# Optimization experiments

Measured on AMD Instinct MI355X. Metric: run time of the kernel, lower is better.

## Reference

```python
import jax, jax.numpy as jnp
import numpy as np

N, E, F_IN, HD, H, G, NG, OUT = 50000, 800000, 128, 64, 4, 512, 50, 64
HC = HD * H  # 256
LN_EPS = 1e-5

def _lin(k, fi, fo):
    return jax.random.normal(k, (fi, fo), jnp.float32) / np.sqrt(fi).astype(np.float32)

def setup_inputs() -> dict:
    key = jax.random.key(0)
    ks = jax.random.split(key, 26)
    x = jax.random.normal(ks[0], (N, F_IN), jnp.float32)
    edge_index = jax.random.randint(ks[1], (2, E), 0, N)
    batch = jnp.sort(jax.random.randint(ks[2], (N,), 0, G))
    group_ids = jax.random.randint(ks[3], (N,), 0, NG)
    inp = {
        'x': x, 'edge_index': edge_index, 'batch': batch, 'group_ids': group_ids,
        'group_table': jax.random.normal(ks[4], (NG, HD), jnp.float32),
        'inW': _lin(ks[5], F_IN + HD, HD), 'inb': jnp.zeros((HD,), jnp.float32),
        'inln_g': jnp.ones((HD,), jnp.float32), 'inln_b': jnp.zeros((HD,), jnp.float32),
        'W0': _lin(ks[6], HD, HC), 'as0': jax.random.normal(ks[7], (H, HD), jnp.float32) * 0.1,
        'ad0': jax.random.normal(ks[8], (H, HD), jnp.float32) * 0.1, 'b0': jnp.zeros((HC,), jnp.float32),
        'ln0g': jnp.ones((HC,), jnp.float32), 'ln0b': jnp.zeros((HC,), jnp.float32),
        'W1': _lin(ks[9], HC, HC), 'as1': jax.random.normal(ks[10], (H, HD), jnp.float32) * 0.1,
        'ad1': jax.random.normal(ks[11], (H, HD), jnp.float32) * 0.1, 'b1': jnp.zeros((HC,), jnp.float32),
        'ln1g': jnp.ones((HC,), jnp.float32), 'ln1b': jnp.zeros((HC,), jnp.float32),
        'fc1W': _lin(ks[12], HC, HD), 'fc1b': jnp.zeros((HD,), jnp.float32),
        'fc2W': _lin(ks[13], HD, OUT), 'fc2b': jnp.zeros((OUT,), jnp.float32),
    }
    return inp

def _layer_norm(x, g, b):
    mu = jnp.mean(x, axis=-1, keepdims=True)
    var = jnp.mean(jnp.square(x - mu), axis=-1, keepdims=True)
    return (x - mu) * jax.lax.rsqrt(var + LN_EPS) * g + b

def _gat_conv(x, src, dst, W, a_src, a_dst, bias):
    # x: [N, Fin] -> per-head projection [N, H, HD]
    xl = (x @ W).reshape(-1, H, HD)
    al_s = jnp.einsum('nhc,hc->nh', xl, a_src)  # [N, H]
    al_d = jnp.einsum('nhc,hc->nh', xl, a_dst)
    e = jax.nn.leaky_relu(al_s[src] + al_d[dst], 0.2)  # [Etot, H]
    m = jax.ops.segment_max(e, dst, num_segments=N)    # stable softmax over in-edges
    ex = jnp.exp(e - m[dst])
    s = jax.ops.segment_sum(ex, dst, num_segments=N)
    alpha = ex / (s[dst] + 1e-16)
    msg = xl[src] * alpha[:, :, None]                   # [Etot, H, HD]
    out = jax.ops.segment_sum(msg, dst, num_segments=N)
    return out.reshape(-1, HC) + bias

def reference(x, edge_index, batch, group_ids, group_table, inW, inb, inln_g, inln_b,
              W0, as0, ad0, b0, ln0g, ln0b, W1, as1, ad1, b1, ln1g, ln1b,
              fc1W, fc1b, fc2W, fc2b):
    # group embedding concat + input projection (Linear -> LN -> GELU)
    h = jnp.concatenate([x, group_table[group_ids]], axis=-1)
    h = jax.nn.gelu(_layer_norm(h @ inW + inb, inln_g, inln_b), approximate=False)
    # add self-loops (PyG GATConv default)
    loop = jnp.arange(N)
    src = jnp.concatenate([edge_index[0], loop])
    dst = jnp.concatenate([edge_index[1], loop])
    # layer 0: dims 64 -> 256, no residual (width mismatch)
    h = jax.nn.gelu(_layer_norm(_gat_conv(h, src, dst, W0, as0, ad0, b0), ln0g, ln0b), approximate=False)
    # layer 1: 256 -> 256, residual applies
    identity = h
    h = jax.nn.gelu(_layer_norm(_gat_conv(h, src, dst, W1, as1, ad1, b1), ln1g, ln1b), approximate=False)
    h = h + identity
    # global mean pool over graphs
    sums = jax.ops.segment_sum(h, batch, num_segments=G)
    cnt = jax.ops.segment_sum(jnp.ones((N, 1), h.dtype), batch, num_segments=G)
    pooled = sums / jnp.maximum(cnt, 1.0)
    z = jax.nn.gelu(pooled @ fc1W + fc1b, approximate=False)
    logits = z @ fc2W + fc2b
    return jax.nn.log_softmax(logits, axis=1)
```

## Files before the change

kernel.cpp:

```cpp
#include <hip/hip_runtime.h>
#include <math.h>

#define N_NODES 50000
#define N_EDGES 800000
#define ETOT (N_EDGES + N_NODES)
#define F_IN 128
#define HD 64
#define NHEAD 4
#define HC 256
#define NGRAPH 512
#define NOUT 64
#define LN_EPS 1e-5f

typedef __attribute__((ext_vector_type(8))) short bf16x8;
typedef __attribute__((ext_vector_type(4))) float f32x4;
typedef __attribute__((ext_vector_type(2))) float f32x2;

__device__ __forceinline__ float wave_sum(float v) {
#pragma unroll
    for (int m = 1; m < 64; m <<= 1) v += __shfl_xor(v, m, 64);
    return v;
}
__device__ __forceinline__ float wave_max(float v) {
#pragma unroll
    for (int m = 1; m < 64; m <<= 1) v = fmaxf(v, __shfl_xor(v, m, 64));
    return v;
}
__device__ __forceinline__ float red16(float v) {
    v += __shfl_xor(v, 1, 64);
    v += __shfl_xor(v, 2, 64);
    v += __shfl_xor(v, 4, 64);
    v += __shfl_xor(v, 8, 64);
    return v;
}
__device__ __forceinline__ float gelu_exact(float x) {
    return 0.5f * x * (1.0f + erff(x * 0.70710678118654752f));
}
__device__ __forceinline__ unsigned short f2bf(float x) {
    unsigned int u = __float_as_uint(x);
    return (unsigned short)((u + 0x7fffu + ((u >> 16) & 1u)) >> 16);
}
__device__ __forceinline__ float bf2f(unsigned short u) {
    return __uint_as_float(((unsigned int)u) << 16);
}

__global__ void k_count(const int* __restrict__ ei, int* __restrict__ deg) {
    int t = blockIdx.x * blockDim.x + threadIdx.x;
    if (t >= ETOT) return;
    int dst = (t < N_EDGES) ? ei[N_EDGES + t] : (t - N_EDGES);
    atomicAdd(deg + dst, 1);
}

__global__ void k_scan(const int* __restrict__ deg, int* __restrict__ rowptr,
                       int* __restrict__ cursor) {
    __shared__ int wsum[16];
    __shared__ int chunk_total;
    int tid = threadIdx.x, wid = tid >> 6, lane = tid & 63;
    int carry = 0;
    if (tid == 0) rowptr[0] = 0;
    for (int base = 0; base < N_NODES; base += 1024) {
        int i = base + tid;
        int v = (i < N_NODES) ? deg[i] : 0;
        int incl = v;
#pragma unroll
        for (int off = 1; off < 64; off <<= 1) {
            int t = __shfl_up(incl, off, 64);
            if (lane >= off) incl += t;
        }
        if (lane == 63) wsum[wid] = incl;
        __syncthreads();
        if (wid == 0) {
            int wv = (lane < 16) ? wsum[lane] : 0;
            int wincl = wv;
#pragma unroll
            for (int off = 1; off < 16; off <<= 1) {
                int t = __shfl_up(wincl, off, 64);
                if (lane >= off) wincl += t;
            }
            if (lane < 16) wsum[lane] = wincl - wv;
            if (lane == 15) chunk_total = wincl;
        }
        __syncthreads();
        int total_incl = carry + wsum[wid] + incl;
        if (i < N_NODES) {
            rowptr[i + 1] = total_incl;
            cursor[i] = total_incl - v;
        }
        carry += chunk_total;
        __syncthreads();
    }
}

__global__ void k_fill(const int* __restrict__ ei, int* __restrict__ cursor,
                       int* __restrict__ csr) {
    int t = blockIdx.x * blockDim.x + threadIdx.x;
    if (t >= ETOT) return;
    int src, dst;
    if (t < N_EDGES) { src = ei[t]; dst = ei[N_EDGES + t]; }
    else             { src = t - N_EDGES; dst = src; }
    int p = atomicAdd(cursor + dst, 1);
    csr[p] = src;
}

__global__ void k_prep(const float* __restrict__ x, const int* __restrict__ gid,
                       const float* __restrict__ gt, unsigned short* __restrict__ Ain) {
    int wid = threadIdx.x >> 6, lane = threadIdx.x & 63;
    int node = blockIdx.x * 4 + wid;
    float f0 = x[node * F_IN + lane];
    float f1 = x[node * F_IN + 64 + lane];
    int g = gid[node];
    float f2 = gt[g * HD + lane];
    unsigned short* r = Ain + (size_t)node * 192;
    r[lane] = f2bf(f0);
    r[64 + lane] = f2bf(f1);
    r[128 + lane] = f2bf(f2);
}

__global__ void k_pack(const float* __restrict__ W, unsigned short* __restrict__ out,
                       int K, int N) {
    int tid = blockIdx.x * blockDim.x + threadIdx.x;
    int NB = N >> 4;
    int total = (K >> 5) * NB * 512;
    if (tid >= total) return;
    int i = tid & 7;
    int l = (tid >> 3) & 63;
    int t2 = tid >> 9;
    int nb = t2 % NB;
    int kt = t2 / NB;
    int k = kt * 32 + ((l >> 4) << 3) + i;
    int n = nb * 16 + (l & 15);
    out[tid] = f2bf(W[k * N + n]);
}

__global__ void k_prep_u(const float* __restrict__ W0, const float* __restrict__ as_,
                         const float* __restrict__ ad_, float* __restrict__ us,
                         float* __restrict__ ud) {
    int t = threadIdx.x;
    int h = t >> 6, k = t & 63;
    float ss = 0.f, dd = 0.f;
    for (int c = 0; c < 64; c++) {
        float w = W0[k * 256 + h * 64 + c];
        ss += w * as_[h * 64 + c];
        dd += w * ad_[h * 64 + c];
    }
    us[t] = ss;
    ud[t] = dd;
}

__global__ void k_proj_in_mma(const unsigned short* __restrict__ A,
                              const unsigned short* __restrict__ Wpk,
                              const float* __restrict__ inb, const float* __restrict__ lng,
                              const float* __restrict__ lnb, const float* __restrict__ us,
                              const float* __restrict__ ud, unsigned short* __restrict__ h0bf,
                              float* __restrict__ als0, float* __restrict__ ald0) {
    int wid = threadIdx.x >> 6, lane = threadIdx.x & 63;
    int m0 = blockIdx.x * 64 + wid * 16;
    if (m0 >= N_NODES) return;
    int g16 = lane >> 4, c16 = lane & 15;
    f32x4 acc[4] = {{0,0,0,0},{0,0,0,0},{0,0,0,0},{0,0,0,0}};
#pragma unroll
    for (int kt = 0; kt < 6; kt++) {
        bf16x8 a = *(const bf16x8*)(A + (size_t)(m0 + c16) * 192 + kt * 32 + g16 * 8);
#pragma unroll
        for (int nt = 0; nt < 4; nt++) {
            bf16x8 b = *(const bf16x8*)(Wpk + (((kt * 4 + nt) * 64 + lane) << 3));
            acc[nt] = __builtin_amdgcn_mfma_f32_16x16x32_bf16(a, b, acc[nt], 0, 0, 0);
        }
    }
    float bv[4], gv[4], bb[4];
    float usl[4][4], udl[4][4];
#pragma unroll
    for (int nt = 0; nt < 4; nt++) {
        int c = nt * 16 + c16;
        bv[nt] = inb[c]; gv[nt] = lng[c]; bb[nt] = lnb[c];
#pragma unroll
        for (int h = 0; h < 4; h++) {
            usl[h][nt] = us[h * 64 + c];
            udl[h][nt] = ud[h * 64 + c];
        }
    }
#pragma unroll
    for (int j = 0; j < 4; j++) {
        float d[4], s = 0.f;
#pragma unroll
        for (int nt = 0; nt < 4; nt++) { d[nt] = acc[nt][j] + bv[nt]; s += d[nt]; }
        float mu = red16(s) * (1.0f / 64.0f);
        float v = 0.f;
#pragma unroll
        for (int nt = 0; nt < 4; nt++) { d[nt] -= mu; v += d[nt] * d[nt]; }
        float r = rsqrtf(red16(v) * (1.0f / 64.0f) + LN_EPS);
        int row = m0 + g16 * 4 + j;
        float ps0 = 0, ps1 = 0, ps2 = 0, ps3 = 0;
        float pd0 = 0, pd1 = 0, pd2 = 0, pd3 = 0;
#pragma unroll
        for (int nt = 0; nt < 4; nt++) {
            float y = gelu_exact(d[nt] * r * gv[nt] + bb[nt]);
            unsigned short yb = f2bf(y);
            h0bf[(size_t)row * 64 + nt * 16 + c16] = yb;
            float yr = bf2f(yb);
            ps0 += yr * usl[0][nt]; ps1 += yr * usl[1][nt];
            ps2 += yr * usl[2][nt]; ps3 += yr * usl[3][nt];
            pd0 += yr * udl[0][nt]; pd1 += yr * udl[1][nt];
            pd2 += yr * udl[2][nt]; pd3 += yr * udl[3][nt];
        }
        ps0 = red16(ps0); ps1 = red16(ps1); ps2 = red16(ps2); ps3 = red16(ps3);
        pd0 = red16(pd0); pd1 = red16(pd1); pd2 = red16(pd2); pd3 = red16(pd3);
        if (c16 == 0) {
            float4 s4 = {ps0, ps1, ps2, ps3};
            float4 d4 = {pd0, pd1, pd2, pd3};
            ((float4*)als0)[row] = s4;
            ((float4*)ald0)[row] = d4;
        }
    }
}

__global__ void k_agg0(const int* __restrict__ rowptr, const int* __restrict__ csr,
                       const unsigned short* __restrict__ h0bf, const float* __restrict__ als,
                       const float* __restrict__ ald, unsigned short* __restrict__ aggbf) {
    __shared__ float4 lacc[2][64];
    __shared__ float lss[2][4];
    int wid = threadIdx.x >> 6, lane = threadIdx.x & 63;
    int nloc = wid >> 1, half = wid & 1;
    int node = blockIdx.x * 2 + nloc;
    int start = rowptr[node], end = rowptr[node + 1];
    int g = lane >> 4, l16 = lane & 15;
    float4 adv = ((const float4*)ald)[node];
    int cntE = end - start;
    int mid = start + ((cntE + 1) >> 1);
    int k0 = half ? mid : start;
    int k1 = half ? end : mid;
    float a00 = 0, a01 = 0, a02 = 0, a03 = 0;
    float a10 = 0, a11 = 0, a12 = 0, a13 = 0;
    float a20 = 0, a21 = 0, a22 = 0, a23 = 0;
    float a30 = 0, a31 = 0, a32 = 0, a33 = 0;
    float s0 = 0, s1 = 0, s2 = 0, s3 = 0;
    const ushort4* h04 = (const ushort4*)h0bf;
    for (int kb = k0; kb < k1; kb += 4) {
        int e = kb + g;
        if (e < k1) {
            int sn = csr[e];
            float4 av = ((const float4*)als)[sn];
            float e0 = av.x + adv.x; e0 = fmaxf(e0, 0.2f * e0);
            float e1 = av.y + adv.y; e1 = fmaxf(e1, 0.2f * e1);
            float e2 = av.z + adv.z; e2 = fmaxf(e2, 0.2f * e2);
            float e3 = av.w + adv.w; e3 = fmaxf(e3, 0.2f * e3);
            float w0 = __expf(e0), w1 = __expf(e1), w2 = __expf(e2), w3 = __expf(e3);
            s0 += w0; s1 += w1; s2 += w2; s3 += w3;
            ushort4 hv = h04[(size_t)sn * 16 + l16];
            float x0 = bf2f(hv.x), x1 = bf2f(hv.y), x2 = bf2f(hv.z), x3 = bf2f(hv.w);
            a00 += w0 * x0; a01 += w0 * x1; a02 += w0 * x2; a03 += w0 * x3;
            a10 += w1 * x0; a11 += w1 * x1; a12 += w1 * x2; a13 += w1 * x3;
            a20 += w2 * x0; a21 += w2 * x1; a22 += w2 * x2; a23 += w2 * x3;
            a30 += w3 * x0; a31 += w3 * x1; a32 += w3 * x2; a33 += w3 * x3;
        }
    }
#define RED2(v) v += __shfl_xor(v, 16, 64); v += __shfl_xor(v, 32, 64)
    RED2(a00); RED2(a01); RED2(a02); RED2(a03);
    RED2(a10); RED2(a11); RED2(a12); RED2(a13);
    RED2(a20); RED2(a21); RED2(a22); RED2(a23);
    RED2(a30); RED2(a31); RED2(a32); RED2(a33);
    RED2(s0);  RED2(s1);  RED2(s2);  RED2(s3);
#undef RED2
    if (half) {
        float o0 = (g == 0) ? a00 : (g == 1) ? a10 : (g == 2) ? a20 : a30;
        float o1 = (g == 0) ? a01 : (g == 1) ? a11 : (g == 2) ? a21 : a31;
        float o2 = (g == 0) ? a02 : (g == 1) ? a12 : (g == 2) ? a22 : a32;
        float o3 = (g == 0) ? a03 : (g == 1) ? a13 : (g == 2) ? a23 : a33;
        float4 o = {o0, o1, o2, o3};
        lacc[nloc][lane] = o;
        if (lane < 4) {
            float sv = (lane == 0) ? s0 : (lane == 1) ? s1 : (lane == 2) ? s2 : s3;
            lss[nloc][lane] = sv;
        }
    }
    __syncthreads();
    if (!half) {
        float4 p0 = lacc[nloc][0 + l16];
        float4 p1 = lacc[nloc][16 + l16];
        float4 p2 = lacc[nloc][32 + l16];
        float4 p3 = lacc[nloc][48 + l16];
        a00 += p0.x; a01 += p0.y; a02 += p0.z; a03 += p0.w;
        a10 += p1.x; a11 += p1.y; a12 += p1.z; a13 += p1.w;
        a20 += p2.x; a21 += p2.y; a22 += p2.z; a23 += p2.w;
        a30 += p3.x; a31 += p3.y; a32 += p3.z; a33 += p3.w;
        s0 += lss[nloc][0]; s1 += lss[nloc][1];
        s2 += lss[nloc][2]; s3 += lss[nloc][3];
        float o0 = (g == 0) ? a00 : (g == 1) ? a10 : (g == 2) ? a20 : a30;
        float o1 = (g == 0) ? a01 : (g == 1) ? a11 : (g == 2) ? a21 : a31;
        float o2 = (g == 0) ? a02 : (g == 1) ? a12 : (g == 2) ? a22 : a32;
        float o3 = (g == 0) ? a03 : (g == 1) ? a13 : (g == 2) ? a23 : a33;
        float sg = (g == 0) ? s0 : (g == 1) ? s1 : (g == 2) ? s2 : s3;
        float inv = 1.0f / (sg + 1e-16f);
        ushort4 o = {f2bf(o0 * inv), f2bf(o1 * inv), f2bf(o2 * inv), f2bf(o3 * inv)};
        ((ushort4*)aggbf)[(size_t)node * 64 + lane] = o;
    }
}

__global__ void k_postgemm0(const unsigned short* __restrict__ A,
                            const unsigned short* __restrict__ Wpk,
                            const float* __restrict__ bias, const float* __restrict__ lng,
                            const float* __restrict__ lnb, unsigned short* __restrict__ h1bf) {
    int wid = threadIdx.x >> 6, lane = threadIdx.x & 63;
    int m0 = blockIdx.x * 64 + wid * 16;
    if (m0 >= N_NODES) return;
    int g16 = lane >> 4, c16 = lane & 15;
    f32x4 acc[16] = {};
#pragma unroll
    for (int h = 0; h < 4; h++) {
#pragma unroll
        for (int kt = 0; kt < 2; kt++) {
            bf16x8 a = *(const bf16x8*)(A + (size_t)(m0 + c16) * 256 + h * 64 + kt * 32 + g16 * 8);
#pragma unroll
            for (int nt = 0; nt < 4; nt++) {
                bf16x8 b = *(const bf16x8*)(Wpk + (((kt * 16 + h * 4 + nt) * 64 + lane) << 3));
                acc[h * 4 + nt] = __builtin_amdgcn_mfma_f32_16x16x32_bf16(a, b, acc[h * 4 + nt], 0, 0, 0);
            }
        }
    }
    float bv[16], gv[16], bb[16];
#pragma unroll
    for (int q = 0; q < 16; q++) {
        int c = q * 16 + c16;
        bv[q] = bias[c]; gv[q] = lng[c]; bb[q] = lnb[c];
    }
#pragma unroll
    for (int j = 0; j < 4; j++) {
        float d[16], ssum = 0.f;
#pragma unroll
        for (int q = 0; q < 16; q++) { d[q] = acc[q][j] + bv[q]; ssum += d[q]; }
        float mu = red16(ssum) * (1.0f / 256.0f);
        float v = 0.f;
#pragma unroll
        for (int q = 0; q < 16; q++) { d[q] -= mu; v += d[q] * d[q]; }
        float r = rsqrtf(red16(v) * (1.0f / 256.0f) + LN_EPS);
        int row = m0 + g16 * 4 + j;
#pragma unroll
        for (int q = 0; q < 16; q++) {
            float y = gelu_exact(d[q] * r * gv[q] + bb[q]);
            h1bf[(size_t)row * 256 + q * 16 + c16] = f2bf(y);
        }
    }
}

__global__ void k_proj_mma(const unsigned short* __restrict__ A,
                           const unsigned short* __restrict__ Wpk,
                           const float* __restrict__ as_, const float* __restrict__ ad_,
                           unsigned int* __restrict__ xl8, float* __restrict__ als,
                           float* __restrict__ ald) {
    int wid = threadIdx.x >> 6, lane = threadIdx.x & 63;
    int m0 = blockIdx.x * 16;
    int g16 = lane >> 4, c16 = lane & 15;
    f32x4 acc[4] = {{0,0,0,0},{0,0,0,0},{0,0,0,0},{0,0,0,0}};
#pragma unroll
    for (int kt = 0; kt < 8; kt++) {
        bf16x8 a = *(const bf16x8*)(A + (size_t)(m0 + c16) * 256 + kt * 32 + g16 * 8);
#pragma unroll
        for (int nt = 0; nt < 4; nt++) {
            bf16x8 b = *(const bf16x8*)(Wpk + (((kt * 16 + wid * 4 + nt) * 64 + lane) << 3));
            acc[nt] = __builtin_amdgcn_mfma_f32_16x16x32_bf16(a, b, acc[nt], 0, 0, 0);
        }
    }
    float asv[4], adv[4];
#pragma unroll
    for (int nt = 0; nt < 4; nt++) {
        int c = wid * 64 + nt * 16 + c16;
        asv[nt] = as_[c]; adv[nt] = ad_[c];
    }
#pragma unroll
    for (int j = 0; j < 4; j++) {
        int row = m0 + g16 * 4 + j;
        float v0 = acc[0][j], v1 = acc[1][j], v2 = acc[2][j], v3 = acc[3][j];
        int u = __builtin_amdgcn_cvt_pk_fp8_f32(v0, v1, 0, false);
        u = __builtin_amdgcn_cvt_pk_fp8_f32(v2, v3, u, true);
        xl8[(size_t)row * 64 + wid * 16 + c16] = (unsigned int)u;
        float ps = v0 * asv[0] + v1 * asv[1] + v2 * asv[2] + v3 * asv[3];
        float pd = v0 * adv[0] + v1 * adv[1] + v2 * adv[2] + v3 * adv[3];
        ps = red16(ps); pd = red16(pd);
        if (c16 == 0) { als[row * 4 + wid] = ps; ald[row * 4 + wid] = pd; }
    }
}

__global__ void k_agg1(const int* __restrict__ rowptr, const int* __restrict__ csr,
                       const unsigned int* __restrict__ xl8, const float* __restrict__ als,
                       const float* __restrict__ ald, const float* __restrict__ bias,
                       const float* __restrict__ lng, const float* __restrict__ lnb,
                       const unsigned short* __restrict__ identity_bf,
                       const int* __restrict__ batch, float* __restrict__ pooled,
                       int* __restrict__ cnt) {
    __shared__ float4 lacc[2][64];
    __shared__ float lss[2][64];
    __shared__ float4 lyout[2][64];
    __shared__ int lbatch[2];
    int wid = threadIdx.x >> 6, lane = threadIdx.x & 63;
    int nloc = wid >> 1, half = wid & 1;
    int node = blockIdx.x * 2 + nloc;
    int start = rowptr[node], end = rowptr[node + 1];
    int head = lane >> 4, c16 = lane & 15;
    int fb = head * 64 + c16;
    float adh = ald[node * 4 + head];
    int cntE = end - start;
    int mid = start + ((cntE + 1) >> 1);
    int k0 = half ? mid : start;
    int k1 = half ? end : mid;
    float4 acc = {0.f, 0.f, 0.f, 0.f};
    float s = 0.f;
    int k = k0;
    for (; k + 4 <= k1; k += 4) {
        int sn0 = csr[k], sn1 = csr[k + 1], sn2 = csr[k + 2], sn3 = csr[k + 3];
        float e0 = als[sn0 * 4 + head] + adh;
        float e1 = als[sn1 * 4 + head] + adh;
        float e2 = als[sn2 * 4 + head] + adh;
        float e3 = als[sn3 * 4 + head] + adh;
        unsigned int u0 = xl8[(size_t)sn0 * 64 + lane];
        unsigned int u1 = xl8[(size_t)sn1 * 64 + lane];
        unsigned int u2 = xl8[(size_t)sn2 * 64 + lane];
        unsigned int u3 = xl8[(size_t)sn3 * 64 + lane];
        e0 = fmaxf(e0, 0.2f * e0); e1 = fmaxf(e1, 0.2f * e1);
        e2 = fmaxf(e2, 0.2f * e2); e3 = fmaxf(e3, 0.2f * e3);
        float a0 = __expf(e0), a1 = __expf(e1), a2 = __expf(e2), a3 = __expf(e3);
        s += a0 + a1 + a2 + a3;
        f32x2 lo0 = __builtin_amdgcn_cvt_pk_f32_fp8((int)u0, false);
        f32x2 hi0 = __builtin_amdgcn_cvt_pk_f32_fp8((int)u0, true);
        f32x2 lo1 = __builtin_amdgcn_cvt_pk_f32_fp8((int)u1, false);
        f32x2 hi1 = __builtin_amdgcn_cvt_pk_f32_fp8((int)u1, true);
        f32x2 lo2 = __builtin_amdgcn_cvt_pk_f32_fp8((int)u2, false);
        f32x2 hi2 = __builtin_amdgcn_cvt_pk_f32_fp8((int)u2, true);
        f32x2 lo3 = __builtin_amdgcn_cvt_pk_f32_fp8((int)u3, false);
        f32x2 hi3 = __builtin_amdgcn_cvt_pk_f32_fp8((int)u3, true);
        acc.x += a0 * lo0.x + a1 * lo1.x + a2 * lo2.x + a3 * lo3.x;
        acc.y += a0 * lo0.y + a1 * lo1.y + a2 * lo2.y + a3 * lo3.y;
        acc.z += a0 * hi0.x + a1 * hi1.x + a2 * hi2.x + a3 * hi3.x;
        acc.w += a0 * hi0.y + a1 * hi1.y + a2 * hi2.y + a3 * hi3.y;
    }
    for (; k < k1; k++) {
        int sn = csr[k];
        float e = als[sn * 4 + head] + adh;
        e = fmaxf(e, 0.2f * e);
        float a = __expf(e);
        s += a;
        unsigned int u = xl8[(size_t)sn * 64 + lane];
        f32x2 lo = __builtin_amdgcn_cvt_pk_f32_fp8((int)u, false);
        f32x2 hi = __builtin_amdgcn_cvt_pk_f32_fp8((int)u, true);
        acc.x += a * lo.x; acc.y += a * lo.y;
        acc.z += a * hi.x; acc.w += a * hi.y;
    }
    if (half) { lacc[nloc][lane] = acc; lss[nloc][lane] = s; }
    __syncthreads();
    if (!half) {
        float4 p = lacc[nloc][lane];
        acc.x += p.x; acc.y += p.y; acc.z += p.z; acc.w += p.w;
        s += lss[nloc][lane];
        float inv = 1.0f / (s + 1e-16f);
        acc.x = acc.x * inv + bias[fb];
        acc.y = acc.y * inv + bias[fb + 16];
        acc.z = acc.z * inv + bias[fb + 32];
        acc.w = acc.w * inv + bias[fb + 48];
        float mu = wave_sum(acc.x + acc.y + acc.z + acc.w) * (1.0f / 256.0f);
        float dx = acc.x - mu, dy = acc.y - mu, dz = acc.z - mu, dw = acc.w - mu;
        float var = wave_sum(dx * dx + dy * dy + dz * dz + dw * dw) * (1.0f / 256.0f);
        float r = rsqrtf(var + LN_EPS);
        float g0v = lng[fb], g1v = lng[fb + 16], g2v = lng[fb + 32], g3v = lng[fb + 48];
        float b0v = lnb[fb], b1v = lnb[fb + 16], b2v = lnb[fb + 32], b3v = lnb[fb + 48];
        const unsigned short* idp = identity_bf + (size_t)node * 256 + fb;
        float4 y;
        y.x = gelu_exact(dx * r * g0v + b0v) + bf2f(idp[0]);
        y.y = gelu_exact(dy * r * g1v + b1v) + bf2f(idp[16]);
        y.z = gelu_exact(dz * r * g2v + b2v) + bf2f(idp[32]);
        y.w = gelu_exact(dw * r * g3v + b3v) + bf2f(idp[48]);
        lyout[nloc][lane] = y;
        if (lane == 0) lbatch[nloc] = batch[node];
    }
    __syncthreads();
    if (wid == 0) {
        int g0 = lbatch[0], g1 = lbatch[1];
        float4 a = lyout[0][lane], b = lyout[1][lane];
        float* p0 = pooled + (size_t)g0 * 256 + fb;
        if (g0 == g1) {
            atomicAdd(p0 +  0, a.x + b.x); atomicAdd(p0 + 16, a.y + b.y);
            atomicAdd(p0 + 32, a.z + b.z); atomicAdd(p0 + 48, a.w + b.w);
            if (lane == 0) atomicAdd(cnt + g0, 2);
        } else {
            float* p1 = pooled + (size_t)g1 * 256 + fb;
            atomicAdd(p0 +  0, a.x); atomicAdd(p0 + 16, a.y);
            atomicAdd(p0 + 32, a.z); atomicAdd(p0 + 48, a.w);
            atomicAdd(p1 +  0, b.x); atomicAdd(p1 + 16, b.y);
            atomicAdd(p1 + 32, b.z); atomicAdd(p1 + 48, b.w);
            if (lane == 0) { atomicAdd(cnt + g0, 1); atomicAdd(cnt + g1, 1); }
        }
    }
}

__global__ void k_final(const float* __restrict__ pooled, const int* __restrict__ cnt,
                        const float* __restrict__ fc1W, const float* __restrict__ fc1b,
                        const float* __restrict__ fc2W, const float* __restrict__ fc2b,
                        float* __restrict__ out) {
    __shared__ float prow[4][256];
    __shared__ float zrow[4][64];
    int wid = threadIdx.x >> 6, lane = threadIdx.x & 63;
    int g = blockIdx.x * 4 + wid;
    float inv = 1.0f / fmaxf((float)cnt[g], 1.0f);
#pragma unroll
    for (int k = lane; k < 256; k += 64) prow[wid][k] = pooled[g * 256 + k] * inv;
    __syncthreads();
    float acc = fc1b[lane];
#pragma unroll 4
    for (int k = 0; k < 256; k++) acc += prow[wid][k] * fc1W[k * 64 + lane];
    zrow[wid][lane] = gelu_exact(acc);
    __syncthreads();
    float logit = fc2b[lane];
#pragma unroll 4
    for (int k = 0; k < 64; k++) logit += zrow[wid][k] * fc2W[k * 64 + lane];
    float mx = wave_max(logit);
    float se = wave_sum(__expf(logit - mx));
    out[g * NOUT + lane] = logit - mx - logf(se);
}

extern "C" void kernel_launch(void* const* d_in, const int* in_sizes, int n_in,
                              void* d_out, int out_size, void* d_ws, size_t ws_size,
                              hipStream_t stream) {
    const float* x     = (const float*)d_in[0];
    const int*   ei    = (const int*)d_in[1];
    const int*   batch = (const int*)d_in[2];
    const int*   gid   = (const int*)d_in[3];
    const float* gt    = (const float*)d_in[4];
    const float* inW   = (const float*)d_in[5];
    const float* inb   = (const float*)d_in[6];
    const float* inlng = (const float*)d_in[7];
    const float* inlnb = (const float*)d_in[8];
    const float* W0    = (const float*)d_in[9];
    const float* as0   = (const float*)d_in[10];
    const float* ad0   = (const float*)d_in[11];
    const float* b0    = (const float*)d_in[12];
    const float* ln0g  = (const float*)d_in[13];
    const float* ln0b  = (const float*)d_in[14];
    const float* W1    = (const float*)d_in[15];
    const float* as1   = (const float*)d_in[16];
    const float* ad1   = (const float*)d_in[17];
    const float* b1    = (const float*)d_in[18];
    const float* ln1g  = (const float*)d_in[19];
    const float* ln1b  = (const float*)d_in[20];
    const float* fc1W  = (const float*)d_in[21];
    const float* fc1b  = (const float*)d_in[22];
    const float* fc2W  = (const float*)d_in[23];
    const float* fc2b  = (const float*)d_in[24];
    float* out = (float*)d_out;

    char* ws = (char*)d_ws;
    size_t off = 0;
    auto alloc = [&](size_t bytes) {
        void* p = ws + off;
        off += (bytes + 255) / 256 * 256;
        return p;
    };
    unsigned short* Ain    = (unsigned short*)alloc((size_t)N_NODES * 192 * 2);
    unsigned short* h0bf   = (unsigned short*)alloc((size_t)N_NODES * 64 * 2);
    unsigned short* agg0bf = (unsigned short*)alloc((size_t)N_NODES * 256 * 2);
    unsigned short* h1bf   = (unsigned short*)alloc((size_t)N_NODES * 256 * 2);
    unsigned int*   xl8    = (unsigned int*)alloc((size_t)N_NODES * 64 * 4);
    unsigned short* inWpk  = (unsigned short*)alloc((size_t)192 * 64 * 2);
    unsigned short* W0pk   = (unsigned short*)alloc((size_t)64 * 256 * 2);
    unsigned short* W1pk   = (unsigned short*)alloc((size_t)256 * 256 * 2);
    float* us     = (float*)alloc((size_t)256 * 4);
    float* ud     = (float*)alloc((size_t)256 * 4);
    float* als0   = (float*)alloc((size_t)N_NODES * 4 * 4);
    float* ald0   = (float*)alloc((size_t)N_NODES * 4 * 4);
    float* als1   = (float*)alloc((size_t)N_NODES * 4 * 4);
    float* ald1   = (float*)alloc((size_t)N_NODES * 4 * 4);
    int*   rowptr = (int*)alloc((size_t)(N_NODES + 1) * 4);
    int*   cursor = (int*)alloc((size_t)N_NODES * 4);
    int*   csr    = (int*)alloc((size_t)ETOT * 4);
    float* pooled = (float*)alloc((size_t)NGRAPH * 256 * 4);
    int*   cnt    = (int*)alloc((size_t)NGRAPH * 4);
    int*   deg    = (int*)alloc((size_t)N_NODES * 4);
    size_t zspan = ((char*)deg + (size_t)N_NODES * 4) - (char*)pooled;

    hipMemsetAsync(pooled, 0, zspan, stream);

    int eb = (ETOT + 255) / 256;
    k_count<<<eb, 256, 0, stream>>>(ei, deg);
    k_scan<<<1, 1024, 0, stream>>>(deg, rowptr, cursor);
    k_fill<<<eb, 256, 0, stream>>>(ei, cursor, csr);

    k_prep<<<N_NODES / 4, 256, 0, stream>>>(x, gid, gt, Ain);
    k_pack<<<(192 * 64 + 255) / 256, 256, 0, stream>>>(inW, inWpk, 192, 64);
    k_pack<<<(64 * 256 + 255) / 256, 256, 0, stream>>>(W0, W0pk, 64, 256);
    k_pack<<<(256 * 256 + 255) / 256, 256, 0, stream>>>(W1, W1pk, 256, 256);
    k_prep_u<<<1, 256, 0, stream>>>(W0, as0, ad0, us, ud);

    k_proj_in_mma<<<(N_NODES + 63) / 64, 256, 0, stream>>>(Ain, inWpk, inb, inlng, inlnb,
                                                           us, ud, h0bf, als0, ald0);
    k_agg0<<<N_NODES / 2, 256, 0, stream>>>(rowptr, csr, h0bf, als0, ald0, agg0bf);
    k_postgemm0<<<(N_NODES + 63) / 64, 256, 0, stream>>>(agg0bf, W0pk, b0, ln0g, ln0b, h1bf);
    k_proj_mma<<<N_NODES / 16, 256, 0, stream>>>(h1bf, W1pk, as1, ad1, xl8, als1, ald1);
    k_agg1<<<N_NODES / 2, 256, 0, stream>>>(rowptr, csr, xl8, als1, ald1, b1, ln1g, ln1b,
                                            h1bf, batch, pooled, cnt);
    k_final<<<NGRAPH / 4, 256, 0, stream>>>(pooled, cnt, fc1W, fc1b, fc2W, fc2b, out);
}
```

Before: 426.4 us.

## Store layer-0 features in fp8, merge weight packing kernels, unroll aggregations

```diff
diff --git a/kernel.cpp b/kernel.cpp
--- a/kernel.cpp
+++ b/kernel.cpp
@@ -116,42 +116,54 @@
     r[128 + lane] = f2bf(f2);
 }
 
-__global__ void k_pack(const float* __restrict__ W, unsigned short* __restrict__ out,
-                       int K, int N) {
-    int tid = blockIdx.x * blockDim.x + threadIdx.x;
-    int NB = N >> 4;
-    int total = (K >> 5) * NB * 512;
-    if (tid >= total) return;
-    int i = tid & 7;
-    int l = (tid >> 3) & 63;
-    int t2 = tid >> 9;
-    int nb = t2 % NB;
-    int kt = t2 / NB;
-    int k = kt * 32 + ((l >> 4) << 3) + i;
-    int n = nb * 16 + (l & 15);
-    out[tid] = f2bf(W[k * N + n]);
-}
-
-__global__ void k_prep_u(const float* __restrict__ W0, const float* __restrict__ as_,
-                         const float* __restrict__ ad_, float* __restrict__ us,
-                         float* __restrict__ ud) {
-    int t = threadIdx.x;
-    int h = t >> 6, k = t & 63;
-    float ss = 0.f, dd = 0.f;
-    for (int c = 0; c < 64; c++) {
-        float w = W0[k * 256 + h * 64 + c];
-        ss += w * as_[h * 64 + c];
-        dd += w * ad_[h * 64 + c];
-    }
-    us[t] = ss;
-    ud[t] = dd;
+__global__ void k_pack_all(const float* __restrict__ inW, const float* __restrict__ W0,
+                           const float* __restrict__ W1, const float* __restrict__ as0,
+                           const float* __restrict__ ad0,
+                           unsigned short* __restrict__ inWpk, unsigned short* __restrict__ W0pk,
+                           unsigned short* __restrict__ W1pk, float* __restrict__ us,
+                           float* __restrict__ ud) {
+    int b = blockIdx.x;
+    if (b < 48) {
+        int tid = b * 256 + threadIdx.x;
+        int i = tid & 7, l = (tid >> 3) & 63, t2 = tid >> 9;
+        int nb = t2 % 4, kt = t2 / 4;
+        int k = kt * 32 + ((l >> 4) << 3) + i;
+        int n = nb * 16 + (l & 15);
+        inWpk[tid] = f2bf(inW[k * 64 + n]);
+    } else if (b < 112) {
+        int tid = (b - 48) * 256 + threadIdx.x;
+        int i = tid & 7, l = (tid >> 3) & 63, t2 = tid >> 9;
+        int nb = t2 % 16, kt = t2 / 16;
+        int q = kt * 32 + ((l >> 4) << 3) + i;
+        int k = 16 * (q & 3) + (q >> 2);
+        int n = nb * 16 + (l & 15);
+        W0pk[tid] = f2bf(W0[k * 256 + n]);
+    } else if (b < 368) {
+        int tid = (b - 112) * 256 + threadIdx.x;
+        int i = tid & 7, l = (tid >> 3) & 63, t2 = tid >> 9;
+        int nb = t2 % 16, kt = t2 / 16;
+        int k = kt * 32 + ((l >> 4) << 3) + i;
+        int n = nb * 16 + (l & 15);
+        W1pk[tid] = f2bf(W1[k * 256 + n]);
+    } else {
+        int t = threadIdx.x;
+        int h = t >> 6, k2 = t & 63;
+        float ss = 0.f, dd = 0.f;
+        for (int c = 0; c < 64; c++) {
+            float w = W0[k2 * 256 + h * 64 + c];
+            ss += w * as0[h * 64 + c];
+            dd += w * ad0[h * 64 + c];
+        }
+        us[t] = ss;
+        ud[t] = dd;
+    }
 }
 
 __global__ void k_proj_in_mma(const unsigned short* __restrict__ A,
                               const unsigned short* __restrict__ Wpk,
                               const float* __restrict__ inb, const float* __restrict__ lng,
                               const float* __restrict__ lnb, const float* __restrict__ us,
-                              const float* __restrict__ ud, unsigned short* __restrict__ h0bf,
+                              const float* __restrict__ ud, unsigned int* __restrict__ h08,
                               float* __restrict__ als0, float* __restrict__ ald0) {
     int wid = threadIdx.x >> 6, lane = threadIdx.x & 63;
     int m0 = blockIdx.x * 64 + wid * 16;
@@ -190,19 +202,21 @@
         for (int nt = 0; nt < 4; nt++) { d[nt] -= mu; v += d[nt] * d[nt]; }
         float r = rsqrtf(red16(v) * (1.0f / 64.0f) + LN_EPS);
         int row = m0 + g16 * 4 + j;
-        float ps0 = 0, ps1 = 0, ps2 = 0, ps3 = 0;
-        float pd0 = 0, pd1 = 0, pd2 = 0, pd3 = 0;
-#pragma unroll
-        for (int nt = 0; nt < 4; nt++) {
-            float y = gelu_exact(d[nt] * r * gv[nt] + bb[nt]);
-            unsigned short yb = f2bf(y);
-            h0bf[(size_t)row * 64 + nt * 16 + c16] = yb;
-            float yr = bf2f(yb);
-            ps0 += yr * usl[0][nt]; ps1 += yr * usl[1][nt];
-            ps2 += yr * usl[2][nt]; ps3 += yr * usl[3][nt];
-            pd0 += yr * udl[0][nt]; pd1 += yr * udl[1][nt];
-            pd2 += yr * udl[2][nt]; pd3 += yr * udl[3][nt];
-        }
+        float y0 = gelu_exact(d[0] * r * gv[0] + bb[0]);
+        float y1 = gelu_exact(d[1] * r * gv[1] + bb[1]);
+        float y2 = gelu_exact(d[2] * r * gv[2] + bb[2]);
+        float y3 = gelu_exact(d[3] * r * gv[3] + bb[3]);
+        int u = __builtin_amdgcn_cvt_pk_fp8_f32(y0, y1, 0, false);
+        u = __builtin_amdgcn_cvt_pk_fp8_f32(y2, y3, u, true);
+        h08[(size_t)row * 16 + c16] = (unsigned int)u;
+        float ps0 = y0 * usl[0][0] + y1 * usl[0][1] + y2 * usl[0][2] + y3 * usl[0][3];
+        float ps1 = y0 * usl[1][0] + y1 * usl[1][1] + y2 * usl[1][2] + y3 * usl[1][3];
+        float ps2 = y0 * usl[2][0] + y1 * usl[2][1] + y2 * usl[2][2] + y3 * usl[2][3];
+        float ps3 = y0 * usl[3][0] + y1 * usl[3][1] + y2 * usl[3][2] + y3 * usl[3][3];
+        float pd0 = y0 * udl[0][0] + y1 * udl[0][1] + y2 * udl[0][2] + y3 * udl[0][3];
+        float pd1 = y0 * udl[1][0] + y1 * udl[1][1] + y2 * udl[1][2] + y3 * udl[1][3];
+        float pd2 = y0 * udl[2][0] + y1 * udl[2][1] + y2 * udl[2][2] + y3 * udl[2][3];
+        float pd3 = y0 * udl[3][0] + y1 * udl[3][1] + y2 * udl[3][2] + y3 * udl[3][3];
         ps0 = red16(ps0); ps1 = red16(ps1); ps2 = red16(ps2); ps3 = red16(ps3);
         pd0 = red16(pd0); pd1 = red16(pd1); pd2 = red16(pd2); pd3 = red16(pd3);
         if (c16 == 0) {
@@ -215,7 +229,7 @@
 }
 
 __global__ void k_agg0(const int* __restrict__ rowptr, const int* __restrict__ csr,
-                       const unsigned short* __restrict__ h0bf, const float* __restrict__ als,
+                       const unsigned int* __restrict__ h08, const float* __restrict__ als,
                        const float* __restrict__ ald, unsigned short* __restrict__ aggbf) {
     __shared__ float4 lacc[2][64];
     __shared__ float lss[2][4];
@@ -234,25 +248,43 @@
     float a20 = 0, a21 = 0, a22 = 0, a23 = 0;
     float a30 = 0, a31 = 0, a32 = 0, a33 = 0;
     float s0 = 0, s1 = 0, s2 = 0, s3 = 0;
-    const ushort4* h04 = (const ushort4*)h0bf;
-    for (int kb = k0; kb < k1; kb += 4) {
-        int e = kb + g;
-        if (e < k1) {
-            int sn = csr[e];
-            float4 av = ((const float4*)als)[sn];
-            float e0 = av.x + adv.x; e0 = fmaxf(e0, 0.2f * e0);
-            float e1 = av.y + adv.y; e1 = fmaxf(e1, 0.2f * e1);
-            float e2 = av.z + adv.z; e2 = fmaxf(e2, 0.2f * e2);
-            float e3 = av.w + adv.w; e3 = fmaxf(e3, 0.2f * e3);
-            float w0 = __expf(e0), w1 = __expf(e1), w2 = __expf(e2), w3 = __expf(e3);
-            s0 += w0; s1 += w1; s2 += w2; s3 += w3;
-            ushort4 hv = h04[(size_t)sn * 16 + l16];
-            float x0 = bf2f(hv.x), x1 = bf2f(hv.y), x2 = bf2f(hv.z), x3 = bf2f(hv.w);
-            a00 += w0 * x0; a01 += w0 * x1; a02 += w0 * x2; a03 += w0 * x3;
-            a10 += w1 * x0; a11 += w1 * x1; a12 += w1 * x2; a13 += w1 * x3;
-            a20 += w2 * x0; a21 += w2 * x1; a22 += w2 * x2; a23 += w2 * x3;
-            a30 += w3 * x0; a31 += w3 * x1; a32 += w3 * x2; a33 += w3 * x3;
-        }
+    const float4* als4 = (const float4*)als;
+    for (int kb = k0; kb < k1; kb += 8) {
+        int eA = kb + g, eB = kb + 4 + g;
+        int cA = (eA < k1) ? eA : (k1 - 1);
+        int cB = (eB < k1) ? eB : (k1 - 1);
+        int snA = csr[cA], snB = csr[cB];
+        float4 avA = als4[snA], avB = als4[snB];
+        unsigned int uA = h08[(size_t)snA * 16 + l16];
+        unsigned int uB = h08[(size_t)snB * 16 + l16];
+        float eA0 = avA.x + adv.x; eA0 = fmaxf(eA0, 0.2f * eA0);
+        float eA1 = avA.y + adv.y; eA1 = fmaxf(eA1, 0.2f * eA1);
+        float eA2 = avA.z + adv.z; eA2 = fmaxf(eA2, 0.2f * eA2);
+        float eA3 = avA.w + adv.w; eA3 = fmaxf(eA3, 0.2f * eA3);
+        float wA0 = __expf(eA0), wA1 = __expf(eA1), wA2 = __expf(eA2), wA3 = __expf(eA3);
+        if (eA >= k1) { wA0 = 0.f; wA1 = 0.f; wA2 = 0.f; wA3 = 0.f; }
+        f32x2 loA = __builtin_amdgcn_cvt_pk_f32_fp8((int)uA, false);
+        f32x2 hiA = __builtin_amdgcn_cvt_pk_f32_fp8((int)uA, true);
+        s0 += wA0; s1 += wA1; s2 += wA2; s3 += wA3;
+        float x0 = loA.x, x1 = loA.y, x2 = hiA.x, x3 = hiA.y;
+        a00 += wA0 * x0; a01 += wA0 * x1; a02 += wA0 * x2; a03 += wA0 * x3;
+        a10 += wA1 * x0; a11 += wA1 * x1; a12 += wA1 * x2; a13 += wA1 * x3;
+        a20 += wA2 * x0; a21 += wA2 * x1; a22 += wA2 * x2; a23 += wA2 * x3;
+        a30 += wA3 * x0; a31 += wA3 * x1; a32 += wA3 * x2; a33 += wA3 * x3;
+        float eB0 = avB.x + adv.x; eB0 = fmaxf(eB0, 0.2f * eB0);
+        float eB1 = avB.y + adv.y; eB1 = fmaxf(eB1, 0.2f * eB1);
+        float eB2 = avB.z + adv.z; eB2 = fmaxf(eB2, 0.2f * eB2);
+        float eB3 = avB.w + adv.w; eB3 = fmaxf(eB3, 0.2f * eB3);
+        float wB0 = __expf(eB0), wB1 = __expf(eB1), wB2 = __expf(eB2), wB3 = __expf(eB3);
+        if (eB >= k1) { wB0 = 0.f; wB1 = 0.f; wB2 = 0.f; wB3 = 0.f; }
+        f32x2 loB = __builtin_amdgcn_cvt_pk_f32_fp8((int)uB, false);
+        f32x2 hiB = __builtin_amdgcn_cvt_pk_f32_fp8((int)uB, true);
+        s0 += wB0; s1 += wB1; s2 += wB2; s3 += wB3;
+        float z0 = loB.x, z1 = loB.y, z2 = hiB.x, z3 = hiB.y;
+        a00 += wB0 * z0; a01 += wB0 * z1; a02 += wB0 * z2; a03 += wB0 * z3;
+        a10 += wB1 * z0; a11 += wB1 * z1; a12 += wB1 * z2; a13 += wB1 * z3;
+        a20 += wB2 * z0; a21 += wB2 * z1; a22 += wB2 * z2; a23 += wB2 * z3;
+        a30 += wB3 * z0; a31 += wB3 * z1; a32 += wB3 * z2; a33 += wB3 * z3;
     }
 #define RED2(v) v += __shfl_xor(v, 16, 64); v += __shfl_xor(v, 32, 64)
     RED2(a00); RED2(a01); RED2(a02); RED2(a03);
@@ -405,6 +437,52 @@
     float4 acc = {0.f, 0.f, 0.f, 0.f};
     float s = 0.f;
     int k = k0;
+    for (; k + 8 <= k1; k += 8) {
+        int sn0 = csr[k],     sn1 = csr[k + 1], sn2 = csr[k + 2], sn3 = csr[k + 3];
+        int sn4 = csr[k + 4], sn5 = csr[k + 5], sn6 = csr[k + 6], sn7 = csr[k + 7];
+        float e0 = als[sn0 * 4 + head], e1 = als[sn1 * 4 + head];
+        float e2 = als[sn2 * 4 + head], e3 = als[sn3 * 4 + head];
+        float e4 = als[sn4 * 4 + head], e5 = als[sn5 * 4 + head];
+        float e6 = als[sn6 * 4 + head], e7 = als[sn7 * 4 + head];
+        unsigned int u0 = xl8[(size_t)sn0 * 64 + lane], u1 = xl8[(size_t)sn1 * 64 + lane];
+        unsigned int u2 = xl8[(size_t)sn2 * 64 + lane], u3 = xl8[(size_t)sn3 * 64 + lane];
+        unsigned int u4 = xl8[(size_t)sn4 * 64 + lane], u5 = xl8[(size_t)sn5 * 64 + lane];
+        unsigned int u6 = xl8[(size_t)sn6 * 64 + lane], u7 = xl8[(size_t)sn7 * 64 + lane];
+        e0 += adh; e1 += adh; e2 += adh; e3 += adh;
+        e0 = fmaxf(e0, 0.2f * e0); e1 = fmaxf(e1, 0.2f * e1);
+        e2 = fmaxf(e2, 0.2f * e2); e3 = fmaxf(e3, 0.2f * e3);
+        float a0 = __expf(e0), a1 = __expf(e1), a2 = __expf(e2), a3 = __expf(e3);
+        s += a0 + a1 + a2 + a3;
+        f32x2 lo0 = __builtin_amdgcn_cvt_pk_f32_fp8((int)u0, false);
+        f32x2 hi0 = __builtin_amdgcn_cvt_pk_f32_fp8((int)u0, true);
+        f32x2 lo1 = __builtin_amdgcn_cvt_pk_f32_fp8((int)u1, false);
+        f32x2 hi1 = __builtin_amdgcn_cvt_pk_f32_fp8((int)u1, true);
+        f32x2 lo2 = __builtin_amdgcn_cvt_pk_f32_fp8((int)u2, false);
+        f32x2 hi2 = __builtin_amdgcn_cvt_pk_f32_fp8((int)u2, true);
+        f32x2 lo3 = __builtin_amdgcn_cvt_pk_f32_fp8((int)u3, false);
+        f32x2 hi3 = __builtin_amdgcn_cvt_pk_f32_fp8((int)u3, true);
+        acc.x += a0 * lo0.x + a1 * lo1.x + a2 * lo2.x + a3 * lo3.x;
+        acc.y += a0 * lo0.y + a1 * lo1.y + a2 * lo2.y + a3 * lo3.y;
+        acc.z += a0 * hi0.x + a1 * hi1.x + a2 * hi2.x + a3 * hi3.x;
+        acc.w += a0 * hi0.y + a1 * hi1.y + a2 * hi2.y + a3 * hi3.y;
+        e4 += adh; e5 += adh; e6 += adh; e7 += adh;
+        e4 = fmaxf(e4, 0.2f * e4); e5 = fmaxf(e5, 0.2f * e5);
+        e6 = fmaxf(e6, 0.2f * e6); e7 = fmaxf(e7, 0.2f * e7);
+        float a4 = __expf(e4), a5 = __expf(e5), a6 = __expf(e6), a7 = __expf(e7);
+        s += a4 + a5 + a6 + a7;
+        f32x2 lo4 = __builtin_amdgcn_cvt_pk_f32_fp8((int)u4, false);
+        f32x2 hi4 = __builtin_amdgcn_cvt_pk_f32_fp8((int)u4, true);
+        f32x2 lo5 = __builtin_amdgcn_cvt_pk_f32_fp8((int)u5, false);
+        f32x2 hi5 = __builtin_amdgcn_cvt_pk_f32_fp8((int)u5, true);
+        f32x2 lo6 = __builtin_amdgcn_cvt_pk_f32_fp8((int)u6, false);
+        f32x2 hi6 = __builtin_amdgcn_cvt_pk_f32_fp8((int)u6, true);
+        f32x2 lo7 = __builtin_amdgcn_cvt_pk_f32_fp8((int)u7, false);
+        f32x2 hi7 = __builtin_amdgcn_cvt_pk_f32_fp8((int)u7, true);
+        acc.x += a4 * lo4.x + a5 * lo5.x + a6 * lo6.x + a7 * lo7.x;
+        acc.y += a4 * lo4.y + a5 * lo5.y + a6 * lo6.y + a7 * lo7.y;
+        acc.z += a4 * hi4.x + a5 * hi5.x + a6 * hi6.x + a7 * hi7.x;
+        acc.w += a4 * hi4.y + a5 * hi5.y + a6 * hi6.y + a7 * hi7.y;
+    }
     for (; k + 4 <= k1; k += 4) {
         int sn0 = csr[k], sn1 = csr[k + 1], sn2 = csr[k + 2], sn3 = csr[k + 3];
         float e0 = als[sn0 * 4 + head] + adh;
@@ -553,7 +631,7 @@
         return p;
     };
     unsigned short* Ain    = (unsigned short*)alloc((size_t)N_NODES * 192 * 2);
-    unsigned short* h0bf   = (unsigned short*)alloc((size_t)N_NODES * 64 * 2);
+    unsigned int*   h08    = (unsigned int*)alloc((size_t)N_NODES * 16 * 4);
     unsigned short* agg0bf = (unsigned short*)alloc((size_t)N_NODES * 256 * 2);
     unsigned short* h1bf   = (unsigned short*)alloc((size_t)N_NODES * 256 * 2);
     unsigned int*   xl8    = (unsigned int*)alloc((size_t)N_NODES * 64 * 4);
@@ -582,14 +660,11 @@
     k_fill<<<eb, 256, 0, stream>>>(ei, cursor, csr);
 
     k_prep<<<N_NODES / 4, 256, 0, stream>>>(x, gid, gt, Ain);
-    k_pack<<<(192 * 64 + 255) / 256, 256, 0, stream>>>(inW, inWpk, 192, 64);
-    k_pack<<<(64 * 256 + 255) / 256, 256, 0, stream>>>(W0, W0pk, 64, 256);
-    k_pack<<<(256 * 256 + 255) / 256, 256, 0, stream>>>(W1, W1pk, 256, 256);
-    k_prep_u<<<1, 256, 0, stream>>>(W0, as0, ad0, us, ud);
+    k_pack_all<<<369, 256, 0, stream>>>(inW, W0, W1, as0, ad0, inWpk, W0pk, W1pk, us, ud);
 
     k_proj_in_mma<<<(N_NODES + 63) / 64, 256, 0, stream>>>(Ain, inWpk, inb, inlng, inlnb,
-                                                           us, ud, h0bf, als0, ald0);
-    k_agg0<<<N_NODES / 2, 256, 0, stream>>>(rowptr, csr, h0bf, als0, ald0, agg0bf);
+                                                           us, ud, h08, als0, ald0);
+    k_agg0<<<N_NODES / 2, 256, 0, stream>>>(rowptr, csr, h08, als0, ald0, agg0bf);
     k_postgemm0<<<(N_NODES + 63) / 64, 256, 0, stream>>>(agg0bf, W0pk, b0, ln0g, ln0b, h1bf);
     k_proj_mma<<<N_NODES / 16, 256, 0, stream>>>(h1bf, W1pk, as1, ad1, xl8, als1, ald1);
     k_agg1<<<N_NODES / 2, 256, 0, stream>>>(rowptr, csr, xl8, als1, ald1, b1, ln1g, ln1b,
```

Result: no change. 420.3 us (-1.4%).
